# Performance work log

Measured on AMD Instinct MI355X. Metric: run time of the kernel, lower is better.

Reference implementation:

```python
import jax, jax.numpy as jnp
import numpy as np

CNN_DIM = 256
CLASS_NUM = 6
NHOPS = 2
ATT_DIM = 50


def conv1d(x, w, b, pad):
    # x: [B, Cin, L], w: [Cout, Cin, K]
    y = jax.lax.conv_general_dilated(x, w, (1,), [(pad, pad)],
                                     dimension_numbers=('NCH', 'OIH', 'NCH'))
    return y + b[None, :, None]


def setup_inputs() -> dict:
    key = jax.random.key(0)
    ks = jax.random.split(key, 16)
    B, L, V, GE, DE = 8, 128, 30000, 300, 100
    IN = GE + DE
    C = CLASS_NUM
    s = 0.02
    inp = {}
    inp['x'] = jax.random.randint(ks[0], (B, L), 0, V)
    inp['x_len'] = L  # python int, stands in for x_len[0] (max length)
    inp['x_mask'] = jnp.ones((B, L), dtype=jnp.float32)
    inp['gen_table'] = jax.random.normal(ks[1], (V, GE), jnp.float32) * s
    inp['domain_table'] = jax.random.normal(ks[2], (V, DE), jnp.float32) * s
    inp['w1'] = jax.random.normal(ks[3], (128, IN, 5)) * s
    inp['b1'] = jnp.zeros((128,))
    inp['w2'] = jax.random.normal(ks[4], (128, IN, 3)) * s
    inp['b2'] = jnp.zeros((128,))
    inp['w3'] = jax.random.normal(ks[5], (256, 256, 5)) * s
    inp['b3'] = jnp.zeros((256,))
    inp['w4'] = jax.random.normal(ks[6], (256, 256, 5)) * s
    inp['b4'] = jnp.zeros((256,))
    inp['w5'] = jax.random.normal(ks[7], (256, 256, 5)) * s
    inp['b5'] = jnp.zeros((256,))
    inp['wq'] = jax.random.normal(ks[8], (CNN_DIM, ATT_DIM)) * s
    inp['bq'] = jnp.zeros((ATT_DIM,))
    inp['wv'] = jax.random.normal(ks[9], (CNN_DIM, ATT_DIM)) * s
    inp['bv'] = jnp.zeros((ATT_DIM,))
    inp['vv'] = jax.random.normal(ks[10], (ATT_DIM,)) * s
    inp['wf'] = jax.random.normal(ks[11], (2 * CNN_DIM + 3 * C, 2 * CNN_DIM)) * s
    inp['bf'] = jnp.zeros((2 * CNN_DIM,))
    inp['wc'] = jax.random.normal(ks[12], (2 * CNN_DIM, C)) * s
    inp['bc'] = jnp.zeros((C,))
    return inp


def reference(x, x_len, x_mask, gen_table, domain_table,
              w1, b1, w2, b2, w3, b3, w4, b4, w5, b5,
              wq, bq, wv, bv, vv, wf, bf, wc, bc):
    # embeddings (dropout omitted: eval mode)
    emb = jnp.concatenate([gen_table[x], domain_table[x]], axis=2)  # [B,L,400]
    xe = jnp.swapaxes(emb, 1, 2)  # [B,400,L]
    xc = jax.nn.relu(jnp.concatenate([conv1d(xe, w1, b1, 2),
                                      conv1d(xe, w2, b2, 1)], axis=1))
    xc = jax.nn.relu(conv1d(xc, w3, b3, 2))
    xc = jax.nn.relu(conv1d(xc, w4, b4, 2))
    xc = jax.nn.relu(conv1d(xc, w5, b5, 2))
    xc = jnp.swapaxes(xc, 1, 2)[:, :x_len, :]  # [B,L,256]
    mask = x_mask[:, :x_len]
    # perceptron (additive) self-attention: v^T tanh(Wq q_i + Wv v_j)
    q = xc @ wq + bq  # [B,L,50]
    v = xc @ wv + bv  # [B,L,50]
    scores = jnp.tanh(q[:, :, None, :] + v[:, None, :, :]) @ vv  # [B,L,L]
    scores = jnp.where(mask[:, None, :] == 0, -1e9, scores)
    attn = jax.nn.softmax(scores, axis=2)
    merged = jnp.einsum('bij,bjd->bid', attn, xc) * mask[:, :, None]
    xc = xc + merged
    B, L, D = xc.shape
    # grid features: (i,j) -> [h_i, h_j]
    features = jnp.concatenate([
        jnp.broadcast_to(xc[:, :, None, :], (B, L, L, D)),
        jnp.broadcast_to(xc[:, None, :, :], (B, L, L, D))], axis=3)  # [B,L,L,512]
    # upper-triangular validity mask on the grid
    m2 = jnp.triu(mask[:, None, :] * mask[:, :, None])[..., None]  # [B,L,L,1]
    logits = features @ wc + bc  # [B,L,L,C]
    for _ in range(NHOPS):
        probs = logits
        lg = probs * m2
        lm = jnp.maximum(jnp.max(lg, axis=1), jnp.max(lg, axis=2))  # [B,L,C]
        row = jnp.broadcast_to(lm[:, :, None, :], (B, L, L, lm.shape[-1]))
        grid = jnp.concatenate([row, jnp.swapaxes(row, 1, 2)], axis=3)  # [B,L,L,2C]
        features = jnp.concatenate([features, grid, probs], axis=3) @ wf + bf
        logits = features @ wc + bc
    return logits
```

## Files before the change

### kernel.cpp

```cpp
#include <hip/hip_runtime.h>
#include <hip/hip_bf16.h>
#include <math.h>

#define LSEQ 128
#define BB 8
#define M_TOK (BB*LSEQ)

struct PreArgs {
    const float* src[5];
    float* dst[5];
    int OC[5], CI[5], K[5];
    const int* x;
    const float4* gen4;
    const float4* dom4;
    float4* emb4;
    const float* wf;
    const float* wc;
    float* Wfc;
};
__global__ __launch_bounds__(256) void stage_kernel(PreArgs a) {
    int y = blockIdx.y;
    if (y < 5) {
        int idx = blockIdx.x * 256 + threadIdx.x;
        int OC = a.OC[y], CI = a.CI[y], K = a.K[y];
        int total = OC * CI * K;
        if (idx >= total) return;
        int k = idx % K;
        int r = idx / K;
        int ci = r % CI;
        int oc = r / CI;
        a.dst[y][(ci * K + k) * OC + oc] = a.src[y][idx];
    } else if (y == 5) {
        int m = blockIdx.x;
        if (m >= M_TOK) return;
        int t = a.x[m];
        int i = threadIdx.x;
        if (i < 100) {
            float4 v = (i < 75) ? a.gen4[t * 75 + i] : a.dom4[t * 25 + (i - 75)];
            a.emb4[m * 100 + i] = v;
        }
    } else {
        int r = blockIdx.x;
        if (r >= 512 || threadIdx.x >= 64) return;
        int l = threadIdx.x;
        float p[6] = {0,0,0,0,0,0};
        const float* row = a.wf + r * 512;
        #pragma unroll
        for (int k = 0; k < 8; ++k) {
            int n = l + 64 * k;
            float v = row[n];
            #pragma unroll
            for (int c = 0; c < 6; ++c) p[c] += v * a.wc[n * 6 + c];
        }
        #pragma unroll
        for (int c = 0; c < 6; ++c)
            for (int off = 32; off >= 1; off >>= 1) p[c] += __shfl_xor(p[c], off, 64);
        if (l == 0) {
            #pragma unroll
            for (int c = 0; c < 6; ++c) a.Wfc[r * 6 + c] = p[c];
        }
    }
}

__global__ __launch_bounds__(256) void conv1_v2(const float* __restrict__ emb,
        const float* __restrict__ w1T, const float* __restrict__ b1,
        const float* __restrict__ w2T, const float* __restrict__ b2,
        float* __restrict__ out,
        const float* __restrict__ wf, const float* __restrict__ bf,
        const float* __restrict__ wc, const float* __restrict__ Wfc,
        float* __restrict__ U) {
    __shared__ float xs[400 * 20];
    int ot = blockIdx.y;
    if (ot == 8) {
        if (threadIdx.x >= 64) return;
        int l = threadIdx.x;
        for (int i = 0; i < 9; ++i) {
            int r = blockIdx.x + 64 * i;
            if (r >= 531) break;
            const float* row = (r < 530) ? (wf + r * 512) : bf;
            float p[12];
            #pragma unroll
            for (int c = 0; c < 12; ++c) p[c] = 0.f;
            #pragma unroll
            for (int k = 0; k < 8; ++k) {
                int n = l + 64 * k;
                float v = row[n];
                #pragma unroll
                for (int c = 0; c < 6; ++c) {
                    p[c]     += v * wc[n * 6 + c];
                    p[c + 6] += v * Wfc[n * 6 + c];
                }
            }
            #pragma unroll
            for (int c = 0; c < 12; ++c)
                for (int off = 32; off >= 1; off >>= 1) p[c] += __shfl_xor(p[c], off, 64);
            if (l == 0) {
                #pragma unroll
                for (int c = 0; c < 12; ++c) U[r * 12 + c] = p[c];
            }
        }
        return;
    }
    int pt = blockIdx.x;
    int b = pt >> 3;
    int l0 = (pt & 7) << 4;
    int tid = threadIdx.x;
    for (int idx = tid; idx < 400 * 20; idx += 256) {
        int p = idx / 400;
        int ci = idx - p * 400;
        int l = l0 - 2 + p;
        float v = 0.f;
        if (l >= 0 && l < LSEQ) v = emb[(b * LSEQ + l) * 400 + ci];
        xs[ci * 20 + p] = v;
    }
    __syncthreads();
    int o = tid & 31;
    int s = tid >> 5;
    float acc[16];
    #pragma unroll
    for (int p = 0; p < 16; ++p) acc[p] = 0.f;
    if (ot < 4) {
        const float* wp = w1T + (s * 50 * 5) * 128 + ot * 32 + o;
        for (int i = 0; i < 50; ++i) {
            const float4* x4 = (const float4*)(xs + (s * 50 + i) * 20);
            float4 A0 = x4[0], A1 = x4[1], A2 = x4[2], A3 = x4[3], A4 = x4[4];
            float xv[20] = {A0.x,A0.y,A0.z,A0.w, A1.x,A1.y,A1.z,A1.w,
                            A2.x,A2.y,A2.z,A2.w, A3.x,A3.y,A3.z,A3.w,
                            A4.x,A4.y,A4.z,A4.w};
            #pragma unroll
            for (int k = 0; k < 5; ++k) {
                float w = wp[k * 128];
                #pragma unroll
                for (int p = 0; p < 16; ++p) acc[p] += w * xv[p + k];
            }
            wp += 640;
        }
    } else {
        const float* wp = w2T + (s * 50 * 3) * 128 + (ot - 4) * 32 + o;
        for (int i = 0; i < 50; ++i) {
            const float4* x4 = (const float4*)(xs + (s * 50 + i) * 20);
            float4 A0 = x4[0], A1 = x4[1], A2 = x4[2], A3 = x4[3], A4 = x4[4];
            float xv[20] = {A0.x,A0.y,A0.z,A0.w, A1.x,A1.y,A1.z,A1.w,
                            A2.x,A2.y,A2.z,A2.w, A3.x,A3.y,A3.z,A3.w,
                            A4.x,A4.y,A4.z,A4.w};
            #pragma unroll
            for (int k = 0; k < 3; ++k) {
                float w = wp[k * 128];
                #pragma unroll
                for (int p = 0; p < 16; ++p) acc[p] += w * xv[p + k + 1];
            }
            wp += 384;
        }
    }
    __syncthreads();
    float* rs = xs;
    #pragma unroll
    for (int p = 0; p < 16; ++p) rs[s * 512 + p * 32 + o] = acc[p];
    __syncthreads();
    #pragma unroll
    for (int r = 0; r < 2; ++r) {
        int idx = r * 256 + tid;
        int p = idx >> 5, oo = idx & 31;
        float sum = 0.f;
        #pragma unroll
        for (int ss = 0; ss < 8; ++ss) sum += rs[ss * 512 + p * 32 + oo];
        float bs = (ot < 4) ? b1[ot * 32 + oo] : b2[(ot - 4) * 32 + oo];
        out[(b * LSEQ + l0 + p) * 256 + ot * 32 + oo] = fmaxf(sum + bs, 0.f);
    }
}

__global__ __launch_bounds__(256) void conv256_v2(const float* __restrict__ in,
        const float* __restrict__ wT, const float* __restrict__ bias,
        float* __restrict__ out) {
    __shared__ float xs[256 * 20];
    int pt = blockIdx.x;
    int b = pt >> 3;
    int l0 = (pt & 7) << 4;
    int ot = blockIdx.y;
    int tid = threadIdx.x;
    for (int idx = tid; idx < 256 * 20; idx += 256) {
        int p = idx >> 8;
        int ci = idx & 255;
        int l = l0 - 2 + p;
        float v = 0.f;
        if (l >= 0 && l < LSEQ) v = in[(b * LSEQ + l) * 256 + ci];
        xs[ci * 20 + p] = v;
    }
    __syncthreads();
    int o = tid & 31;
    int s = tid >> 5;
    int oc0 = ot * 32;
    float acc[16];
    #pragma unroll
    for (int p = 0; p < 16; ++p) acc[p] = 0.f;
    const float* wp = wT + (s * 32 * 5) * 256 + oc0 + o;
    for (int i = 0; i < 32; ++i) {
        const float4* x4 = (const float4*)(xs + (s * 32 + i) * 20);
        float4 A0 = x4[0], A1 = x4[1], A2 = x4[2], A3 = x4[3], A4 = x4[4];
        float xv[20] = {A0.x,A0.y,A0.z,A0.w, A1.x,A1.y,A1.z,A1.w,
                        A2.x,A2.y,A2.z,A2.w, A3.x,A3.y,A3.z,A3.w,
                        A4.x,A4.y,A4.z,A4.w};
        #pragma unroll
        for (int k = 0; k < 5; ++k) {
            float w = wp[k * 256];
            #pragma unroll
            for (int p = 0; p < 16; ++p) acc[p] += w * xv[p + k];
        }
        wp += 1280;
    }
    __syncthreads();
    float* rs = xs;
    #pragma unroll
    for (int p = 0; p < 16; ++p) rs[s * 512 + p * 32 + o] = acc[p];
    __syncthreads();
    #pragma unroll
    for (int r = 0; r < 2; ++r) {
        int idx = r * 256 + tid;
        int p = idx >> 5, oo = idx & 31;
        float sum = 0.f;
        #pragma unroll
        for (int ss = 0; ss < 8; ++ss) sum += rs[ss * 512 + p * 32 + oo];
        out[(b * LSEQ + l0 + p) * 256 + oc0 + oo] = fmaxf(sum + bias[oc0 + oo], 0.f);
    }
}

__global__ __launch_bounds__(128) void qv_v2(const float* __restrict__ xc,
        const float* __restrict__ wq, const float* __restrict__ bq,
        const float* __restrict__ wv, const float* __restrict__ bv,
        float* __restrict__ q, float* __restrict__ v) {
    int m = blockIdx.x;
    int tid = threadIdx.x;
    int w = tid >> 6, d = tid & 63;
    if (d >= 50) return;
    const float* W = w ? wv : wq;
    float a = w ? bv[d] : bq[d];
    const float* xm = xc + m * 256;
    #pragma unroll 8
    for (int c = 0; c < 256; ++c) a += xm[c] * W[c * 50 + d];
    (w ? v : q)[m * 50 + d] = a;
}

__global__ __launch_bounds__(256) void attn_v2(const float* __restrict__ xc,
        const float* __restrict__ q, const float* __restrict__ v,
        const float* __restrict__ vv, const float* __restrict__ xmask,
        const float* __restrict__ wc, const float* __restrict__ bc,
        float* __restrict__ xc2, float* __restrict__ f0, float* __restrict__ g0) {
    __shared__ float vs[128 * 50];
    __shared__ float spart[128], aarr[128], xrow[256], qrow[52], vvs[52], red[4];
    int bi = blockIdx.x;
    int b = bi >> 7;
    int tid = threadIdx.x;
    for (int idx = tid; idx < 128 * 50; idx += 256) vs[idx] = v[b * 6400 + idx];
    if (tid < 50) { qrow[tid] = q[bi * 50 + tid]; vvs[tid] = vv[tid]; }
    __syncthreads();
    int j = tid & 127, half = tid >> 7;
    int d0 = half * 25;
    const float* vj = vs + j * 50 + d0;
    float s = 0.f;
    #pragma unroll
    for (int d = 0; d < 25; ++d) {
        float x = qrow[d0 + d] + vj[d];
        float e = __expf(2.f * x);
        s += (1.f - 2.f / (e + 1.f)) * vvs[d0 + d];
    }
    if (half) spart[j] = s;
    __syncthreads();
    float stot = 0.f;
    if (!half) {
        stot = s + spart[j];
        if (xmask[b * LSEQ + j] == 0.f) stot = -1e9f;
    }
    if (tid < 128) {
        float m = stot;
        #pragma unroll
        for (int off = 32; off >= 1; off >>= 1) m = fmaxf(m, __shfl_xor(m, off, 64));
        if ((tid & 63) == 0) red[tid >> 6] = m;
    }
    __syncthreads();
    float mx = fmaxf(red[0], red[1]);
    float e = 0.f;
    if (tid < 128) {
        e = __expf(stot - mx);
        float su = e;
        #pragma unroll
        for (int off = 32; off >= 1; off >>= 1) su += __shfl_xor(su, off, 64);
        if ((tid & 63) == 0) red[2 + (tid >> 6)] = su;
    }
    __syncthreads();
    float denom = red[2] + red[3];
    if (tid < 128) aarr[j] = e / denom;
    __syncthreads();
    float maskI = xmask[bi];
    const float* xcb = xc + b * LSEQ * 256;
    float acc = 0.f;
    #pragma unroll 8
    for (int jj = 0; jj < 128; ++jj) acc += aarr[jj] * xcb[jj * 256 + tid];
    float val = xc[bi * 256 + tid] + acc * maskI;
    xc2[bi * 256 + tid] = val;
    xrow[tid] = val;
    __syncthreads();
    int grp = tid >> 4, l16 = tid & 15;
    if (grp < 12) {
        int c = grp % 6, gsel = grp / 6;
        const float* wcc = wc + gsel * 256 * 6 + c;
        float a = 0.f;
        #pragma unroll
        for (int ch = l16; ch < 256; ch += 16) a += xrow[ch] * wcc[ch * 6];
        #pragma unroll
        for (int off = 8; off >= 1; off >>= 1) a += __shfl_down(a, off, 16);
        if (l16 == 0) {
            if (gsel == 0) f0[bi * 6 + c] = a + bc[c];
            else           g0[bi * 6 + c] = a;
        }
    }
}

__global__ __launch_bounds__(128) void lm_scan_v3(const float* __restrict__ f,
        const float* __restrict__ g, int stride, float* __restrict__ lm) {
    __shared__ float sf[128], sg[128];
    int bc = blockIdx.x;
    int b = bc / 6, c = bc - b * 6;
    int p = threadIdx.x;
    float fv = f[(b * LSEQ + p) * stride + c];
    float gv = g[(b * LSEQ + p) * stride + c];
    sf[p] = fv; sg[p] = gv;
    __syncthreads();
    float pf = fv, sgx = gv;
    #pragma unroll
    for (int off = 1; off < 128; off <<= 1) {
        float a = (p >= off) ? sf[p - off] : -INFINITY;
        float d = (p + off < 128) ? sg[p + off] : -INFINITY;
        __syncthreads();
        pf = fmaxf(pf, a); sgx = fmaxf(sgx, d);
        sf[p] = pf; sg[p] = sgx;
        __syncthreads();
    }
    float M1 = pf + gv;
    if (p < LSEQ - 1) M1 = fmaxf(M1, 0.f);
    float M2 = fv + sgx;
    if (p > 0) M2 = fmaxf(M2, 0.f);
    lm[(b * LSEQ + p) * 6 + c] = fmaxf(M1, M2);
}

__global__ __launch_bounds__(64) void hopfold_kernel(const float* __restrict__ xc2,
        const float* __restrict__ U, const float* __restrict__ lm0,
        const float* __restrict__ f0, const float* __restrict__ g0,
        const float* __restrict__ bc,
        float* __restrict__ outF, float* __restrict__ outG) {
    int m = blockIdx.x;
    int y = blockIdx.y;
    int tid = threadIdx.x;
    const float* Urows = U + (y ? 256 : 0) * 12;
    float p[12];
    #pragma unroll
    for (int c = 0; c < 12; ++c) p[c] = 0.f;
    for (int k = tid; k < 256; k += 64) {
        float a = xc2[m * 256 + k];
        const float* ur = Urows + k * 12;
        #pragma unroll
        for (int c = 0; c < 12; ++c) p[c] += a * ur[c];
    }
    #pragma unroll
    for (int c = 0; c < 12; ++c)
        for (int off = 32; off >= 1; off >>= 1) p[c] += __shfl_xor(p[c], off, 64);
    if (tid == 0) {
        const float* Bb = U + (y ? 518 : 512) * 12;
        const float* Db = U + 524 * 12;
        const float* fg = y ? g0 : f0;
        float* out = y ? outG : outF;
        float lmv[6], fgv[6];
        #pragma unroll
        for (int j = 0; j < 6; ++j) { lmv[j] = lm0[m * 6 + j]; fgv[j] = fg[m * 6 + j]; }
        #pragma unroll
        for (int c = 0; c < 12; ++c) {
            float s = p[c];
            #pragma unroll
            for (int j = 0; j < 6; ++j) s += lmv[j] * Bb[j * 12 + c] + fgv[j] * Db[j * 12 + c];
            if (!y) { s += U[530 * 12 + c]; if (c < 6) s += bc[c]; }
            out[m * 12 + c] = s;
        }
    }
}

__global__ __launch_bounds__(128) void f2g2_kernel(const float* __restrict__ f1phi,
        const float* __restrict__ g1gam, const float* __restrict__ lm1,
        const float* __restrict__ U, const float* __restrict__ bc,
        float* __restrict__ f2, float* __restrict__ g2) {
    __shared__ float Us[19 * 12], bcs[6];
    int tid = threadIdx.x;
    for (int i = tid; i < 19 * 12; i += 128) Us[i] = U[512 * 12 + i];
    if (tid < 6) bcs[tid] = bc[tid];
    __syncthreads();
    int m = blockIdx.x * 128 + tid;
    float lmv[6], f1v[6], g1v[6];
    #pragma unroll
    for (int j = 0; j < 6; ++j) {
        lmv[j] = lm1[m * 6 + j];
        f1v[j] = f1phi[m * 12 + j];
        g1v[j] = g1gam[m * 12 + j];
    }
    #pragma unroll
    for (int c = 0; c < 6; ++c) {
        float sf = f1phi[m * 12 + 6 + c] + Us[18 * 12 + c] + bcs[c];
        float sg = g1gam[m * 12 + 6 + c];
        #pragma unroll
        for (int j = 0; j < 6; ++j) {
            sf += lmv[j] * Us[j * 12 + c]       + f1v[j] * Us[(12 + j) * 12 + c];
            sg += lmv[j] * Us[(6 + j) * 12 + c] + g1v[j] * Us[(12 + j) * 12 + c];
        }
        f2[m * 6 + c] = sf;
        g2[m * 6 + c] = sg;
    }
}

__global__ __launch_bounds__(256) void writeout_kernel(const float* __restrict__ f2,
        const float* __restrict__ g2, float* __restrict__ out) {
    int idx = blockIdx.x * 256 + threadIdx.x;
    int c = idx % 6;
    int r = idx / 6;
    int j = r & 127;
    int bi = r >> 7;
    int b = bi >> 7;
    out[idx] = f2[bi * 6 + c] + g2[(b * LSEQ + j) * 6 + c];
}

extern "C" void kernel_launch(void* const* d_in, const int* in_sizes, int n_in,
                              void* d_out, int out_size, void* d_ws, size_t ws_size,
                              hipStream_t stream) {
    const int*   x     = (const int*)d_in[0];
    const float* xmask = (const float*)d_in[2];
    const float* gen   = (const float*)d_in[3];
    const float* dom   = (const float*)d_in[4];
    const float* w1    = (const float*)d_in[5];
    const float* b1    = (const float*)d_in[6];
    const float* w2    = (const float*)d_in[7];
    const float* b2    = (const float*)d_in[8];
    const float* w3    = (const float*)d_in[9];
    const float* b3    = (const float*)d_in[10];
    const float* w4    = (const float*)d_in[11];
    const float* b4    = (const float*)d_in[12];
    const float* w5    = (const float*)d_in[13];
    const float* b5    = (const float*)d_in[14];
    const float* wq    = (const float*)d_in[15];
    const float* bq    = (const float*)d_in[16];
    const float* wv    = (const float*)d_in[17];
    const float* bv    = (const float*)d_in[18];
    const float* vv    = (const float*)d_in[19];
    const float* wf    = (const float*)d_in[20];
    const float* bf    = (const float*)d_in[21];
    const float* wc    = (const float*)d_in[22];
    const float* bc    = (const float*)d_in[23];

    float* ws = (float*)d_ws;
    float* emb   = ws;
    float* bufA  = emb   + 409600;
    float* bufB  = bufA  + 262144;
    float* xc2   = bufB  + 262144;
    float* qb    = xc2   + 262144;
    float* vb    = qb    + 51200;
    float* w1T   = vb    + 51200;
    float* w2T   = w1T   + 256000;
    float* w3T   = w2T   + 153600;
    float* w4T   = w3T   + 327680;
    float* w5T   = w4T   + 327680;
    float* Wfc   = w5T   + 327680;
    float* U     = Wfc   + 3072;
    float* f0    = U     + 6372;
    float* g0    = f0    + 6144;
    float* lm0   = g0    + 6144;
    float* lm1   = lm0   + 6144;
    float* f1phi = lm1   + 6144;
    float* g1gam = f1phi + 12288;
    float* f2    = g1gam + 12288;
    float* g2    = f2    + 6144;

    PreArgs pa;
    pa.src[0] = w1;  pa.dst[0] = w1T; pa.OC[0] = 128; pa.CI[0] = 400; pa.K[0] = 5;
    pa.src[1] = w2;  pa.dst[1] = w2T; pa.OC[1] = 128; pa.CI[1] = 400; pa.K[1] = 3;
    pa.src[2] = w3;  pa.dst[2] = w3T; pa.OC[2] = 256; pa.CI[2] = 256; pa.K[2] = 5;
    pa.src[3] = w4;  pa.dst[3] = w4T; pa.OC[3] = 256; pa.CI[3] = 256; pa.K[3] = 5;
    pa.src[4] = w5;  pa.dst[4] = w5T; pa.OC[4] = 256; pa.CI[4] = 256; pa.K[4] = 5;
    pa.x = x; pa.gen4 = (const float4*)gen; pa.dom4 = (const float4*)dom;
    pa.emb4 = (float4*)emb;
    pa.wf = wf; pa.wc = wc; pa.Wfc = Wfc;
    stage_kernel<<<dim3(1280, 7), 256, 0, stream>>>(pa);

    conv1_v2<<<dim3(64, 9), 256, 0, stream>>>(emb, w1T, b1, w2T, b2, bufA,
                                              wf, bf, wc, Wfc, U);
    conv256_v2<<<dim3(64, 8), 256, 0, stream>>>(bufA, w3T, b3, bufB);
    conv256_v2<<<dim3(64, 8), 256, 0, stream>>>(bufB, w4T, b4, bufA);
    conv256_v2<<<dim3(64, 8), 256, 0, stream>>>(bufA, w5T, b5, bufB);

    qv_v2<<<M_TOK, 128, 0, stream>>>(bufB, wq, bq, wv, bv, qb, vb);
    attn_v2<<<M_TOK, 256, 0, stream>>>(bufB, qb, vb, vv, xmask, wc, bc, xc2, f0, g0);

    lm_scan_v3<<<48, 128, 0, stream>>>(f0, g0, 6, lm0);
    hopfold_kernel<<<dim3(M_TOK, 2), 64, 0, stream>>>(xc2, U, lm0, f0, g0, bc, f1phi, g1gam);
    lm_scan_v3<<<48, 128, 0, stream>>>(f1phi, g1gam, 12, lm1);
    f2g2_kernel<<<8, 128, 0, stream>>>(f1phi, g1gam, lm1, U, bc, f2, g2);

    writeout_kernel<<<(BB*LSEQ*LSEQ*6)/256, 256, 0, stream>>>(f2, g2, (float*)d_out);
}
```

Baseline: 261.8 us.

## Run conv layers on bf16 MFMA with hi/lo split for fp32-level accuracy

Replaces the scalar FP32 convolution kernels with MFMA-based implicit-GEMM kernels. Activations and weights are split into high and low bf16 parts, and three MFMA products are summed to get close to fp32 accuracy. The staging kernel now converts the weights and the embeddings into bf16 hi/lo tiles laid out for MFMA operand loads. The cost is extra conversion work and three times the MFMA count, plus a change in rounding behaviour compared with pure FP32.

```diff
diff --git a/kernel.cpp b/kernel.cpp
--- a/kernel.cpp
+++ b/kernel.cpp
@@ -1,48 +1,90 @@
 #include <hip/hip_runtime.h>
-#include <hip/hip_bf16.h>
 #include <math.h>
 
 #define LSEQ 128
 #define BB 8
 #define M_TOK (BB*LSEQ)
 
+typedef __attribute__((ext_vector_type(8))) short short8;
+typedef __attribute__((ext_vector_type(4))) float floatx4;
+
+__device__ __forceinline__ unsigned short bf16_rne(float v) {
+    union { float f; unsigned u; } a; a.f = v;
+    return (unsigned short)((a.u + 0x7fffu + ((a.u >> 16) & 1u)) >> 16);
+}
+__device__ __forceinline__ float bf16_to_f(unsigned short h) {
+    union { unsigned u; float f; } b; b.u = ((unsigned)h) << 16;
+    return b.f;
+}
+__device__ __forceinline__ void split2(float v, unsigned short& h, unsigned short& l) {
+    h = bf16_rne(v);
+    l = bf16_rne(v - bf16_to_f(h));
+}
+
 struct PreArgs {
-    const float* src[5];
-    float* dst[5];
-    int OC[5], CI[5], K[5];
+    const float *w1, *w2, *w3, *w4, *w5;
+    unsigned short *B1h, *B1l, *B2h, *B2l, *B3h, *B3l, *B4h, *B4l, *B5h, *B5l;
     const int* x;
-    const float4* gen4;
-    const float4* dom4;
-    float4* emb4;
+    const float* gen;
+    const float* dom;
+    unsigned short *Eh, *El;
     const float* wf;
     const float* wc;
     float* Wfc;
 };
 __global__ __launch_bounds__(256) void stage_kernel(PreArgs a) {
     int y = blockIdx.y;
-    if (y < 5) {
-        int idx = blockIdx.x * 256 + threadIdx.x;
-        int OC = a.OC[y], CI = a.CI[y], K = a.K[y];
-        int total = OC * CI * K;
-        if (idx >= total) return;
-        int k = idx % K;
-        int r = idx / K;
-        int ci = r % CI;
-        int oc = r / CI;
-        a.dst[y][(ci * K + k) * OC + oc] = a.src[y][idx];
+    int tid = threadIdx.x;
+    if (y < 3) {
+        const float* w = (y == 0) ? a.w3 : (y == 1) ? a.w4 : a.w5;
+        unsigned short* dh = (y == 0) ? a.B3h : (y == 1) ? a.B4h : a.B5h;
+        unsigned short* dl = (y == 0) ? a.B3l : (y == 1) ? a.B4l : a.B5l;
+        int idx = blockIdx.x * 256 + tid;
+        int j = idx & 7;
+        int n = (idx >> 3) & 255;
+        int g = idx >> 11;
+        int cg = g & 31, kk = g >> 5;
+        int ci = cg * 8 + j;
+        float v = w[(n * 256 + ci) * 5 + kk];
+        unsigned short h, l; split2(v, h, l);
+        dh[idx] = h; dl[idx] = l;
+    } else if (y == 3) {
+        int idx = blockIdx.x * 256 + tid;
+        if (idx >= 5 * 52 * 128 * 8) return;
+        int j = idx & 7;
+        int n = (idx >> 3) & 127;
+        int g = idx >> 10;
+        int cg = g % 52, kk = g / 52;
+        int ci = cg * 8 + j;
+        float v = (ci < 400) ? a.w1[(n * 400 + ci) * 5 + kk] : 0.f;
+        unsigned short h, l; split2(v, h, l);
+        a.B1h[idx] = h; a.B1l[idx] = l;
+    } else if (y == 4) {
+        int idx = blockIdx.x * 256 + tid;
+        if (idx >= 3 * 52 * 128 * 8) return;
+        int j = idx & 7;
+        int n = (idx >> 3) & 127;
+        int g = idx >> 10;
+        int cg = g % 52, kk = g / 52;
+        int ci = cg * 8 + j;
+        float v = (ci < 400) ? a.w2[(n * 400 + ci) * 3 + kk] : 0.f;
+        unsigned short h, l; split2(v, h, l);
+        a.B2h[idx] = h; a.B2l[idx] = l;
     } else if (y == 5) {
         int m = blockIdx.x;
         if (m >= M_TOK) return;
         int t = a.x[m];
-        int i = threadIdx.x;
-        if (i < 100) {
-            float4 v = (i < 75) ? a.gen4[t * 75 + i] : a.dom4[t * 25 + (i - 75)];
-            a.emb4[m * 100 + i] = v;
+        for (int c = tid; c < 416; c += 256) {
+            float v = (c < 300) ? a.gen[t * 300 + c]
+                    : (c < 400) ? a.dom[t * 100 + (c - 300)] : 0.f;
+            unsigned short h, l; split2(v, h, l);
+            a.Eh[m * 416 + c] = h;
+            a.El[m * 416 + c] = l;
         }
     } else {
         int r = blockIdx.x;
-        if (r >= 512 || threadIdx.x >= 64) return;
-        int l = threadIdx.x;
+        if (r >= 512 || tid >= 64) return;
+        int l = tid;
         float p[6] = {0,0,0,0,0,0};
         const float* row = a.wf + r * 512;
         #pragma unroll
@@ -62,18 +104,22 @@
     }
 }
 
-__global__ __launch_bounds__(256) void conv1_v2(const float* __restrict__ emb,
-        const float* __restrict__ w1T, const float* __restrict__ b1,
-        const float* __restrict__ w2T, const float* __restrict__ b2,
-        float* __restrict__ out,
+__global__ __launch_bounds__(256) void conv1_mfma(
+        const unsigned short* __restrict__ Eh, const unsigned short* __restrict__ El,
+        const unsigned short* __restrict__ B1h, const unsigned short* __restrict__ B1l,
+        const unsigned short* __restrict__ B2h, const unsigned short* __restrict__ B2l,
+        const float* __restrict__ b1, const float* __restrict__ b2,
+        unsigned short* __restrict__ Xoh, unsigned short* __restrict__ Xol,
         const float* __restrict__ wf, const float* __restrict__ bf,
         const float* __restrict__ wc, const float* __restrict__ Wfc,
         float* __restrict__ U) {
-    __shared__ float xs[400 * 20];
-    int ot = blockIdx.y;
-    if (ot == 8) {
-        if (threadIdx.x >= 64) return;
-        int l = threadIdx.x;
+    __shared__ __align__(16) unsigned short xsh[20 * 424];
+    __shared__ __align__(16) unsigned short xsl[20 * 424];
+    int by = blockIdx.y;
+    int tid = threadIdx.x;
+    if (by == 4) {
+        if (tid >= 64) return;
+        int l = tid;
         for (int i = 0; i < 9; ++i) {
             int r = blockIdx.x + 64 * i;
             if (r >= 531) break;
@@ -101,126 +147,145 @@
         }
         return;
     }
-    int pt = blockIdx.x;
-    int b = pt >> 3;
-    int l0 = (pt & 7) << 4;
-    int tid = threadIdx.x;
-    for (int idx = tid; idx < 400 * 20; idx += 256) {
-        int p = idx / 400;
-        int ci = idx - p * 400;
-        int l = l0 - 2 + p;
-        float v = 0.f;
-        if (l >= 0 && l < LSEQ) v = emb[(b * LSEQ + l) * 400 + ci];
-        xs[ci * 20 + p] = v;
-    }
-    __syncthreads();
-    int o = tid & 31;
-    int s = tid >> 5;
-    float acc[16];
-    #pragma unroll
-    for (int p = 0; p < 16; ++p) acc[p] = 0.f;
-    if (ot < 4) {
-        const float* wp = w1T + (s * 50 * 5) * 128 + ot * 32 + o;
-        for (int i = 0; i < 50; ++i) {
-            const float4* x4 = (const float4*)(xs + (s * 50 + i) * 20);
-            float4 A0 = x4[0], A1 = x4[1], A2 = x4[2], A3 = x4[3], A4 = x4[4];
-            float xv[20] = {A0.x,A0.y,A0.z,A0.w, A1.x,A1.y,A1.z,A1.w,
-                            A2.x,A2.y,A2.z,A2.w, A3.x,A3.y,A3.z,A3.w,
-                            A4.x,A4.y,A4.z,A4.w};
-            #pragma unroll
-            for (int k = 0; k < 5; ++k) {
-                float w = wp[k * 128];
-                #pragma unroll
-                for (int p = 0; p < 16; ++p) acc[p] += w * xv[p + k];
+    int mt = blockIdx.x;
+    int p0 = mt * 16;
+    int b = p0 >> 7, l0 = p0 & 127;
+    for (int i = tid; i < 2 * 1040; i += 256) {
+        int sel = i >= 1040;
+        int u2 = sel ? i - 1040 : i;
+        int j = u2 / 52, cg = u2 % 52;
+        int l = l0 - 2 + j;
+        short8 v = {0,0,0,0,0,0,0,0};
+        if (l >= 0 && l < 128) {
+            const unsigned short* src = (sel ? El : Eh) + (b * 128 + l) * 416 + cg * 8;
+            v = *(const short8*)src;
+        }
+        *(short8*)((sel ? xsl : xsh) + j * 424 + cg * 8) = v;
+    }
+    __syncthreads();
+    int w = tid >> 6, lane = tid & 63;
+    int m = lane & 15, q = lane >> 4;
+    bool br2 = (by >= 2);
+    int n0b = (by & 1) * 64;
+    int nB = n0b + w * 16 + m;
+    floatx4 acc0 = {0,0,0,0}, acc1 = {0,0,0,0}, acc2 = {0,0,0,0};
+    if (!br2) {
+        for (int kk = 0; kk < 5; ++kk) {
+            const unsigned short* arh = xsh + (m + kk) * 424;
+            const unsigned short* arl = xsl + (m + kk) * 424;
+            #pragma unroll
+            for (int u = 0; u < 13; ++u) {
+                short8 ah = *(const short8*)(arh + u * 32 + q * 8);
+                short8 al = *(const short8*)(arl + u * 32 + q * 8);
+                int boff = (((kk * 52 + u * 4 + q) * 128) + nB) * 8;
+                short8 bh = *(const short8*)(B1h + boff);
+                short8 bl = *(const short8*)(B1l + boff);
+                acc0 = __builtin_amdgcn_mfma_f32_16x16x32_bf16(ah, bh, acc0, 0, 0, 0);
+                acc1 = __builtin_amdgcn_mfma_f32_16x16x32_bf16(ah, bl, acc1, 0, 0, 0);
+                acc2 = __builtin_amdgcn_mfma_f32_16x16x32_bf16(al, bh, acc2, 0, 0, 0);
             }
-            wp += 640;
         }
     } else {
-        const float* wp = w2T + (s * 50 * 3) * 128 + (ot - 4) * 32 + o;
-        for (int i = 0; i < 50; ++i) {
-            const float4* x4 = (const float4*)(xs + (s * 50 + i) * 20);
-            float4 A0 = x4[0], A1 = x4[1], A2 = x4[2], A3 = x4[3], A4 = x4[4];
-            float xv[20] = {A0.x,A0.y,A0.z,A0.w, A1.x,A1.y,A1.z,A1.w,
-                            A2.x,A2.y,A2.z,A2.w, A3.x,A3.y,A3.z,A3.w,
-                            A4.x,A4.y,A4.z,A4.w};
-            #pragma unroll
-            for (int k = 0; k < 3; ++k) {
-                float w = wp[k * 128];
-                #pragma unroll
-                for (int p = 0; p < 16; ++p) acc[p] += w * xv[p + k + 1];
+        for (int kk = 0; kk < 3; ++kk) {
+            const unsigned short* arh = xsh + (m + kk + 1) * 424;
+            const unsigned short* arl = xsl + (m + kk + 1) * 424;
+            #pragma unroll
+            for (int u = 0; u < 13; ++u) {
+                short8 ah = *(const short8*)(arh + u * 32 + q * 8);
+                short8 al = *(const short8*)(arl + u * 32 + q * 8);
+                int boff = (((kk * 52 + u * 4 + q) * 128) + nB) * 8;
+                short8 bh = *(const short8*)(B2h + boff);
+                short8 bl = *(const short8*)(B2l + boff);
+                acc0 = __builtin_amdgcn_mfma_f32_16x16x32_bf16(ah, bh, acc0, 0, 0, 0);
+                acc1 = __builtin_amdgcn_mfma_f32_16x16x32_bf16(ah, bl, acc1, 0, 0, 0);
+                acc2 = __builtin_amdgcn_mfma_f32_16x16x32_bf16(al, bh, acc2, 0, 0, 0);
             }
-            wp += 384;
-        }
-    }
-    __syncthreads();
-    float* rs = xs;
-    #pragma unroll
-    for (int p = 0; p < 16; ++p) rs[s * 512 + p * 32 + o] = acc[p];
-    __syncthreads();
-    #pragma unroll
-    for (int r = 0; r < 2; ++r) {
-        int idx = r * 256 + tid;
-        int p = idx >> 5, oo = idx & 31;
-        float sum = 0.f;
-        #pragma unroll
-        for (int ss = 0; ss < 8; ++ss) sum += rs[ss * 512 + p * 32 + oo];
-        float bs = (ot < 4) ? b1[ot * 32 + oo] : b2[(ot - 4) * 32 + oo];
-        out[(b * LSEQ + l0 + p) * 256 + ot * 32 + oo] = fmaxf(sum + bs, 0.f);
-    }
-}
-
-__global__ __launch_bounds__(256) void conv256_v2(const float* __restrict__ in,
-        const float* __restrict__ wT, const float* __restrict__ bias,
-        float* __restrict__ out) {
-    __shared__ float xs[256 * 20];
-    int pt = blockIdx.x;
-    int b = pt >> 3;
-    int l0 = (pt & 7) << 4;
-    int ot = blockIdx.y;
-    int tid = threadIdx.x;
-    for (int idx = tid; idx < 256 * 20; idx += 256) {
-        int p = idx >> 8;
-        int ci = idx & 255;
-        int l = l0 - 2 + p;
-        float v = 0.f;
-        if (l >= 0 && l < LSEQ) v = in[(b * LSEQ + l) * 256 + ci];
-        xs[ci * 20 + p] = v;
-    }
-    __syncthreads();
-    int o = tid & 31;
-    int s = tid >> 5;
-    int oc0 = ot * 32;
-    float acc[16];
-    #pragma unroll
-    for (int p = 0; p < 16; ++p) acc[p] = 0.f;
-    const float* wp = wT + (s * 32 * 5) * 256 + oc0 + o;
-    for (int i = 0; i < 32; ++i) {
-        const float4* x4 = (const float4*)(xs + (s * 32 + i) * 20);
-        float4 A0 = x4[0], A1 = x4[1], A2 = x4[2], A3 = x4[3], A4 = x4[4];
-        float xv[20] = {A0.x,A0.y,A0.z,A0.w, A1.x,A1.y,A1.z,A1.w,
-                        A2.x,A2.y,A2.z,A2.w, A3.x,A3.y,A3.z,A3.w,
-                        A4.x,A4.y,A4.z,A4.w};
-        #pragma unroll
-        for (int k = 0; k < 5; ++k) {
-            float w = wp[k * 256];
-            #pragma unroll
-            for (int p = 0; p < 16; ++p) acc[p] += w * xv[p + k];
-        }
-        wp += 1280;
-    }
-    __syncthreads();
-    float* rs = xs;
-    #pragma unroll
-    for (int p = 0; p < 16; ++p) rs[s * 512 + p * 32 + o] = acc[p];
-    __syncthreads();
-    #pragma unroll
-    for (int r = 0; r < 2; ++r) {
-        int idx = r * 256 + tid;
-        int p = idx >> 5, oo = idx & 31;
-        float sum = 0.f;
-        #pragma unroll
-        for (int ss = 0; ss < 8; ++ss) sum += rs[ss * 512 + p * 32 + oo];
-        out[(b * LSEQ + l0 + p) * 256 + oc0 + oo] = fmaxf(sum + bias[oc0 + oo], 0.f);
+        }
+    }
+    __syncthreads();
+    float* fl = (float*)xsh;
+    #pragma unroll
+    for (int reg = 0; reg < 4; ++reg)
+        fl[(q * 4 + reg) * 68 + w * 16 + m] = acc0[reg] + acc1[reg] + acc2[reg];
+    __syncthreads();
+    int ocb = br2 ? 128 + n0b : n0b;
+    const float* bias = br2 ? b2 : b1;
+    #pragma unroll
+    for (int i = 0; i < 4; ++i) {
+        int e = tid + 256 * i;
+        int mm = e >> 6, nn = e & 63;
+        float val = fl[mm * 68 + nn] + bias[n0b + nn];
+        val = fmaxf(val, 0.f);
+        unsigned short h, l; split2(val, h, l);
+        int o = (p0 + mm) * 256 + ocb + nn;
+        Xoh[o] = h; Xol[o] = l;
+    }
+}
+
+__global__ __launch_bounds__(256) void conv256_mfma(
+        const unsigned short* __restrict__ Xih, const unsigned short* __restrict__ Xil,
+        const unsigned short* __restrict__ Bh, const unsigned short* __restrict__ Bl,
+        const float* __restrict__ bias, int outmode,
+        unsigned short* __restrict__ Xoh, unsigned short* __restrict__ Xol,
+        float* __restrict__ fout) {
+    __shared__ __align__(16) unsigned short xsh[20 * 264];
+    __shared__ __align__(16) unsigned short xsl[20 * 264];
+    int mt = blockIdx.x;
+    int p0 = mt * 16;
+    int b = p0 >> 7, l0 = p0 & 127;
+    int n0 = blockIdx.y * 64;
+    int tid = threadIdx.x;
+    for (int i = tid; i < 2 * 640; i += 256) {
+        int sel = i >= 640;
+        int u2 = sel ? i - 640 : i;
+        int j = u2 >> 5, cg = u2 & 31;
+        int l = l0 - 2 + j;
+        short8 v = {0,0,0,0,0,0,0,0};
+        if (l >= 0 && l < 128) {
+            const unsigned short* src = (sel ? Xil : Xih) + (b * 128 + l) * 256 + cg * 8;
+            v = *(const short8*)src;
+        }
+        *(short8*)((sel ? xsl : xsh) + j * 264 + cg * 8) = v;
+    }
+    __syncthreads();
+    int w = tid >> 6, lane = tid & 63;
+    int m = lane & 15, q = lane >> 4;
+    int nB = n0 + w * 16 + m;
+    floatx4 acc0 = {0,0,0,0}, acc1 = {0,0,0,0}, acc2 = {0,0,0,0};
+    for (int kk = 0; kk < 5; ++kk) {
+        const unsigned short* arh = xsh + (m + kk) * 264;
+        const unsigned short* arl = xsl + (m + kk) * 264;
+        #pragma unroll
+        for (int u = 0; u < 8; ++u) {
+            short8 ah = *(const short8*)(arh + u * 32 + q * 8);
+            short8 al = *(const short8*)(arl + u * 32 + q * 8);
+            int boff = (((kk * 32 + u * 4 + q) * 256) + nB) * 8;
+            short8 bh = *(const short8*)(Bh + boff);
+            short8 bl = *(const short8*)(Bl + boff);
+            acc0 = __builtin_amdgcn_mfma_f32_16x16x32_bf16(ah, bh, acc0, 0, 0, 0);
+        acc1 = __builtin_amdgcn_mfma_f32_16x16x32_bf16(ah, bl, acc1, 0, 0, 0);
+            acc2 = __builtin_amdgcn_mfma_f32_16x16x32_bf16(al, bh, acc2, 0, 0, 0);
+        }
+    }
+    __syncthreads();
+    float* fl = (float*)xsh;
+    #pragma unroll
+    for (int reg = 0; reg < 4; ++reg)
+        fl[(q * 4 + reg) * 68 + w * 16 + m] = acc0[reg] + acc1[reg] + acc2[reg];
+    __syncthreads();
+    #pragma unroll
+    for (int i = 0; i < 4; ++i) {
+        int e = tid + 256 * i;
+        int mm = e >> 6, nn = e & 63;
+        float val = fl[mm * 68 + nn] + bias[n0 + nn];
+        val = fmaxf(val, 0.f);
+        int o = (p0 + mm) * 256 + n0 + nn;
+        if (outmode == 0) {
+            unsigned short h, l; split2(val, h, l);
+            Xoh[o] = h; Xol[o] = l;
+        } else {
+            fout[o] = val;
+        }
     }
 }
 
@@ -451,21 +516,14 @@
     const float* wc    = (const float*)d_in[22];
     const float* bc    = (const float*)d_in[23];
 
-    float* ws = (float*)d_ws;
-    float* emb   = ws;
-    float* bufA  = emb   + 409600;
-    float* bufB  = bufA  + 262144;
+    float* fb = (float*)d_ws;
+    float* bufB  = fb;
     float* xc2   = bufB  + 262144;
     float* qb    = xc2   + 262144;
     float* vb    = qb    + 51200;
-    float* w1T   = vb    + 51200;
-    float* w2T   = w1T   + 256000;
-    float* w3T   = w2T   + 153600;
-    float* w4T   = w3T   + 327680;
-    float* w5T   = w4T   + 327680;
-    float* Wfc   = w5T   + 327680;
+    float* Wfc   = vb    + 51200;
     float* U     = Wfc   + 3072;
-    float* f0    = U     + 6372;
+    float* f0    = U     + 6376;
     float* g0    = f0    + 6144;
     float* lm0   = g0    + 6144;
     float* lm1   = lm0   + 6144;
@@ -473,23 +531,41 @@
     float* g1gam = f1phi + 12288;
     float* f2    = g1gam + 12288;
     float* g2    = f2    + 6144;
+    unsigned short* sb = (unsigned short*)(g2 + 6144 + 32);
+    unsigned short* Eh  = sb;             sb += 425984;
+    unsigned short* El  = sb;             sb += 425984;
+    unsigned short* B1h = sb;             sb += 266240;
+    unsigned short* B1l = sb;             sb += 266240;
+    unsigned short* B2h = sb;             sb += 159744;
+    unsigned short* B2l = sb;             sb += 159744;
+    unsigned short* B3h = sb;             sb += 327680;
+    unsigned short* B3l = sb;             sb += 327680;
+    unsigned short* B4h = sb;             sb += 327680;
+    unsigned short* B4l = sb;             sb += 327680;
+    unsigned short* B5h = sb;             sb += 327680;
+    unsigned short* B5l = sb;             sb += 327680;
+    unsigned short* X3h = sb;             sb += 262144;
+    unsigned short* X3l = sb;             sb += 262144;
+    unsigned short* X4h = sb;             sb += 262144;
+    unsigned short* X4l = sb;             sb += 262144;
 
     PreArgs pa;
-    pa.src[0] = w1;  pa.dst[0] = w1T; pa.OC[0] = 128; pa.CI[0] = 400; pa.K[0] = 5;
-    pa.src[1] = w2;  pa.dst[1] = w2T; pa.OC[1] = 128; pa.CI[1] = 400; pa.K[1] = 3;
-    pa.src[2] = w3;  pa.dst[2] = w3T; pa.OC[2] = 256; pa.CI[2] = 256; pa.K[2] = 5;
-    pa.src[3] = w4;  pa.dst[3] = w4T; pa.OC[3] = 256; pa.CI[3] = 256; pa.K[3] = 5;
-    pa.src[4] = w5;  pa.dst[4] = w5T; pa.OC[4] = 256; pa.CI[4] = 256; pa.K[4] = 5;
-    pa.x = x; pa.gen4 = (const float4*)gen; pa.dom4 = (const float4*)dom;
-    pa.emb4 = (float4*)emb;
+    pa.w1 = w1; pa.w2 = w2; pa.w3 = w3; pa.w4 = w4; pa.w5 = w5;
+    pa.B1h = B1h; pa.B1l = B1l; pa.B2h = B2h; pa.B2l = B2l;
+    pa.B3h = B3h; pa.B3l = B3l; pa.B4h = B4h; pa.B4l = B4l;
+    pa.B5h = B5h; pa.B5l = B5l;
+    pa.x = x; pa.gen = gen; pa.dom = dom; pa.Eh = Eh; pa.El = El;
     pa.wf = wf; pa.wc = wc; pa.Wfc = Wfc;
     stage_kernel<<<dim3(1280, 7), 256, 0, stream>>>(pa);
 
-    conv1_v2<<<dim3(64, 9), 256, 0, stream>>>(emb, w1T, b1, w2T, b2, bufA,
-                                              wf, bf, wc, Wfc, U);
-    conv256_v2<<<dim3(64, 8), 256, 0, stream>>>(bufA, w3T, b3, bufB);
-    conv256_v2<<<dim3(64, 8), 256, 0, stream>>>(bufB, w4T, b4, bufA);
-    conv256_v2<<<dim3(64, 8), 256, 0, stream>>>(bufA, w5T, b5, bufB);
+    conv1_mfma<<<dim3(64, 5), 256, 0, stream>>>(Eh, El, B1h, B1l, B2h, B2l, b1, b2,
+                                                X3h, X3l, wf, bf, wc, Wfc, U);
+    conv256_mfma<<<dim3(64, 4), 256, 0, stream>>>(X3h, X3l, B3h, B3l, b3, 0,
+                                                  X4h, X4l, nullptr);
+    conv256_mfma<<<dim3(64, 4), 256, 0, stream>>>(X4h, X4l, B4h, B4l, b4, 0,
+                                                  X3h, X3l, nullptr);
+    conv256_mfma<<<dim3(64, 4), 256, 0, stream>>>(X3h, X3l, B5h, B5l, b5, 1,
+                                                  nullptr, nullptr, bufB);
 
     qv_v2<<<M_TOK, 128, 0, stream>>>(bufB, wq, bq, wv, bv, qb, vb);
     attn_v2<<<M_TOK, 256, 0, stream>>>(bufB, qb, vb, vv, xmask, wc, bc, xc2, f0, g0);
```

After: 241.0 us. 7.9% less time.
